# Kernel optimization log

Hardware: AMD Instinct MI355X
Metric: run time of the kernel (lower is better)

## Reference

```python
import jax, jax.numpy as jnp
import numpy as np

NEG = -1e30  # acts as -inf for logcumsumexp but keeps grads finite


def setup_inputs() -> dict:
    key = jax.random.key(0)
    k1, k2, k3 = jax.random.split(key, 3)
    B, N, L = 2048, 8192, 512
    y_pred_scores = jax.random.normal(k1, (B, N), dtype=jnp.float32)
    idx = jax.random.randint(k2, (B, L), 0, N)
    # ragged valid lengths in [L//2, L]; positions >= length are padded with -1
    lengths = jax.random.randint(k3, (B, 1), L // 2, L + 1)
    pos = jnp.arange(L)[None, :]
    y_true_seqs = jnp.where(pos < lengths, idx, -1).astype(jnp.int64)
    return {"y_pred_scores": y_pred_scores, "y_true_seqs": y_true_seqs}


def reference(y_pred_scores, y_true_seqs):
    # sanitize (torch_sanitize)
    s = jnp.nan_to_num(y_pred_scores, nan=0.0, posinf=1e6, neginf=-1e6)
    mask = y_true_seqs != -1                      # [B, L]
    idx = jnp.clip(y_true_seqs, 0, s.shape[1] - 1)
    g = jnp.take_along_axis(s, idx, axis=1)       # [B, L] gathered scores
    # Removing padded entries then flip+logcumsumexp+flip == suffix logsumexp
    # over the sequence with padded positions contributing exp(NEG)=0.
    gm = jnp.where(mask, g, NEG)
    log_den = jax.lax.cumlogsumexp(gm[:, ::-1], axis=1)[:, ::-1]  # [B, L]
    ll = jnp.where(mask, g - log_den, 0.0).sum(axis=1)            # [B]
    used = jnp.any(mask, axis=1)                                  # [B]
    total_ll = jnp.where(used, ll, 0.0).sum()
    n_used = used.sum().astype(s.dtype)
    return jnp.where(n_used > 0, -total_ll / n_used, jnp.zeros((), s.dtype))
```

## Files before the change

kernel.cpp:

```cpp
#include <hip/hip_runtime.h>

#define NEGV (-1e30f)

__global__ __launch_bounds__(256) void listnet_row_kernel(
    const float* __restrict__ scores,
    const int*   __restrict__ seqs,
    float2*      __restrict__ part,
    int N, int L)
{
    const int b = blockIdx.x;
    const float* srow = scores + (size_t)b * N;
    const int2*  irow = (const int2*)(seqs + (size_t)b * L);

    const int t    = threadIdx.x;
    const int lane = t & 63;
    const int wv   = t >> 6;

    int2 ii = irow[t];
    bool v0 = (ii.x != -1), v1 = (ii.y != -1);
    int  c0 = min(max(ii.x, 0), N - 1);
    int  c1 = min(max(ii.y, 0), N - 1);
    float g0 = srow[c0];
    float g1 = srow[c1];
    g0 = isnan(g0) ? 0.f : fminf(fmaxf(g0, -1e6f), 1e6f);
    g1 = isnan(g1) ? 0.f : fminf(fmaxf(g1, -1e6f), 1e6f);
    float x0 = v0 ? g0 : NEGV;
    float x1 = v1 ? g1 : NEGV;

    float mx = fmaxf(x0, x1);
    #pragma unroll
    for (int off = 32; off; off >>= 1)
        mx = fmaxf(mx, __shfl_xor(mx, off, 64));
    __shared__ float wmax[4];
    if (lane == 0) wmax[wv] = mx;
    __syncthreads();
    const float M = fmaxf(fmaxf(wmax[0], wmax[1]), fmaxf(wmax[2], wmax[3]));

    float e0 = __expf(x0 - M);
    float e1 = __expf(x1 - M);
    float S  = e0 + e1;
    #pragma unroll
    for (int off = 1; off < 64; off <<= 1) {
        float o = __shfl_down(S, off, 64);
        S += (lane + off < 64) ? o : 0.f;
    }
    __shared__ float wtot[4];
    if (lane == 0) wtot[wv] = S;
    float Safter = __shfl_down(S, 1, 64);
    if (lane == 63) Safter = 0.f;
    __syncthreads();
    float above = 0.f;
    if (wv < 3) above += wtot[wv + 1];
    if (wv < 2) above += wtot[wv + 2];
    if (wv < 1) above += wtot[wv + 3];
    const float A = Safter + above;

    float s1 = e1 + A;
    float s0 = e0 + s1;
    float ll = 0.f;
    if (v1) ll += x1 - (M + __logf(s1));
    if (v0) ll += x0 - (M + __logf(s0));

    #pragma unroll
    for (int off = 32; off; off >>= 1)
        ll += __shfl_down(ll, off, 64);
    __shared__ float lsum[4];
    if (lane == 0) lsum[wv] = ll;
    __syncthreads();
    if (t == 0) {
        bool used = (M > -1e29f);
        float2 r;
        r.x = used ? (lsum[0] + lsum[1] + lsum[2] + lsum[3]) : 0.f;
        r.y = used ? 1.f : 0.f;
        part[b] = r;
    }
}

__global__ __launch_bounds__(64) void listnet_finalize_kernel(
    const float2* __restrict__ part, float* __restrict__ out, int B)
{
    const int t = threadIdx.x;
    float tot = 0.f, cnt = 0.f;
    for (int i = t; i < B; i += 64) {
        float2 p = part[i];
        tot += p.x;
        cnt += p.y;
    }
    #pragma unroll
    for (int off = 32; off; off >>= 1) {
        tot += __shfl_down(tot, off, 64);
        cnt += __shfl_down(cnt, off, 64);
    }
    if (t == 0)
        out[0] = (cnt > 0.f) ? (-tot / cnt) : 0.f;
}

extern "C" void kernel_launch(void* const* d_in, const int* in_sizes, int n_in,
                              void* d_out, int out_size, void* d_ws, size_t ws_size,
                              hipStream_t stream) {
    const float* scores = (const float*)d_in[0];
    const int*   seqs   = (const int*)d_in[1];
    float*       out    = (float*)d_out;
    float2*      part   = (float2*)d_ws;

    const int L = 512;
    const int B = in_sizes[1] / L;
    const int N = in_sizes[0] / B;

    listnet_row_kernel<<<B, 256, 0, stream>>>(scores, seqs, part, N, L);
    listnet_finalize_kernel<<<1, 64, 0, stream>>>(part, out, B);
}
```

Baseline: 100.4 us.

## Process one row per wavefront and fuse finalize via last-block atomic counter

Each wavefront now handles a whole row with 8 elements per lane, so the block-level shared-memory reductions and __syncthreads barriers go away and only wave shuffles remain. The separate finalize kernel is replaced by an atomic counter: the last wave to finish reduces the partial results and writes the output. This removes one kernel launch but adds a hipMemsetAsync to reset the counter and puts the serial tail reduction inside the main kernel. The workload is gather-latency bound, so any gain depends on whether fewer barriers and more independent loads per thread improve latency hiding.

```diff
diff --git a/kernel.cpp b/kernel.cpp
--- a/kernel.cpp
+++ b/kernel.cpp
@@ -2,97 +2,99 @@
 
 #define NEGV (-1e30f)
 
-__global__ __launch_bounds__(256) void listnet_row_kernel(
+__global__ __launch_bounds__(256) void listnet_fused_kernel(
     const float* __restrict__ scores,
     const int*   __restrict__ seqs,
     float2*      __restrict__ part,
-    int N, int L)
+    int*         __restrict__ counter,
+    float*       __restrict__ out,
+    int N, int L, int B)
 {
-    const int b = blockIdx.x;
-    const float* srow = scores + (size_t)b * N;
-    const int2*  irow = (const int2*)(seqs + (size_t)b * L);
+    const int lane = threadIdx.x & 63;
+    const int wv   = threadIdx.x >> 6;
+    const int row  = blockIdx.x * 4 + wv;
+    if (row >= B) return;
 
-    const int t    = threadIdx.x;
-    const int lane = t & 63;
-    const int wv   = t >> 6;
+    const float* srow  = scores + (size_t)row * N;
+    const int4*  irow4 = (const int4*)(seqs + (size_t)row * L);
 
-    int2 ii = irow[t];
-    bool v0 = (ii.x != -1), v1 = (ii.y != -1);
-    int  c0 = min(max(ii.x, 0), N - 1);
-    int  c1 = min(max(ii.y, 0), N - 1);
-    float g0 = srow[c0];
-    float g1 = srow[c1];
-    g0 = isnan(g0) ? 0.f : fminf(fmaxf(g0, -1e6f), 1e6f);
-    g1 = isnan(g1) ? 0.f : fminf(fmaxf(g1, -1e6f), 1e6f);
-    float x0 = v0 ? g0 : NEGV;
-    float x1 = v1 ? g1 : NEGV;
+    int4 ia = irow4[lane * 2];
+    int4 ib = irow4[lane * 2 + 1];
+    int idx[8] = {ia.x, ia.y, ia.z, ia.w, ib.x, ib.y, ib.z, ib.w};
 
-    float mx = fmaxf(x0, x1);
+    float x[8];
+    float mloc = NEGV;
+    #pragma unroll
+    for (int j = 0; j < 8; ++j) {
+        bool v = (idx[j] != -1);
+        int  c = min(max(idx[j], 0), N - 1);
+        float g = srow[c];
+        g = isnan(g) ? 0.f : fminf(fmaxf(g, -1e6f), 1e6f);
+        x[j] = v ? g : NEGV;
+        mloc = fmaxf(mloc, x[j]);
+    }
+
+    float M = mloc;
     #pragma unroll
     for (int off = 32; off; off >>= 1)
-        mx = fmaxf(mx, __shfl_xor(mx, off, 64));
-    __shared__ float wmax[4];
-    if (lane == 0) wmax[wv] = mx;
-    __syncthreads();
-    const float M = fmaxf(fmaxf(wmax[0], wmax[1]), fmaxf(wmax[2], wmax[3]));
+        M = fmaxf(M, __shfl_xor(M, off, 64));
 
-    float e0 = __expf(x0 - M);
-    float e1 = __expf(x1 - M);
-    float S  = e0 + e1;
+    float suf[8];
+    float run = 0.f;
+    #pragma unroll
+    for (int j = 7; j >= 0; --j) {
+        run += __expf(x[j] - M);
+        suf[j] = run;
+    }
+
+    float S = run;
     #pragma unroll
     for (int off = 1; off < 64; off <<= 1) {
         float o = __shfl_down(S, off, 64);
         S += (lane + off < 64) ? o : 0.f;
     }
-    __shared__ float wtot[4];
-    if (lane == 0) wtot[wv] = S;
-    float Safter = __shfl_down(S, 1, 64);
-    if (lane == 63) Safter = 0.f;
-    __syncthreads();
-    float above = 0.f;
-    if (wv < 3) above += wtot[wv + 1];
-    if (wv < 2) above += wtot[wv + 2];
-    if (wv < 1) above += wtot[wv + 3];
-    const float A = Safter + above;
+    float A = __shfl_down(S, 1, 64);
+    if (lane == 63) A = 0.f;
 
-    float s1 = e1 + A;
-    float s0 = e0 + s1;
     float ll = 0.f;
-    if (v1) ll += x1 - (M + __logf(s1));
-    if (v0) ll += x0 - (M + __logf(s0));
-
+    #pragma unroll
+    for (int j = 0; j < 8; ++j) {
+        if (idx[j] != -1)
+            ll += x[j] - (M + __logf(suf[j] + A));
+    }
     #pragma unroll
     for (int off = 32; off; off >>= 1)
         ll += __shfl_down(ll, off, 64);
-    __shared__ float lsum[4];
-    if (lane == 0) lsum[wv] = ll;
-    __syncthreads();
-    if (t == 0) {
+
+    int old = 0;
+    if (lane == 0) {
         bool used = (M > -1e29f);
         float2 r;
-        r.x = used ? (lsum[0] + lsum[1] + lsum[2] + lsum[3]) : 0.f;
+        r.x = used ? ll : 0.f;
         r.y = used ? 1.f : 0.f;
-        part[b] = r;
+        part[row] = r;
+        __threadfence();
+        old = atomicAdd(counter, 1);
     }
-}
+    old = __shfl(old, 0, 64);
 
-__global__ __launch_bounds__(64) void listnet_finalize_kernel(
-    const float2* __restrict__ part, float* __restrict__ out, int B)
-{
-    const int t = threadIdx.x;
-    float tot = 0.f, cnt = 0.f;
-    for (int i = t; i < B; i += 64) {
-        float2 p = part[i];
-        tot += p.x;
-        cnt += p.y;
+    if (old == B - 1) {
+        __threadfence();
+        const volatile float2* vp = (const volatile float2*)part;
+        float tot = 0.f, cnt = 0.f;
+        for (int i = lane; i < B; i += 64) {
+            float2 p; p.x = vp[i].x; p.y = vp[i].y;
+            tot += p.x;
+            cnt += p.y;
+        }
+        #pragma unroll
+        for (int off = 32; off; off >>= 1) {
+            tot += __shfl_down(tot, off, 64);
+            cnt += __shfl_down(cnt, off, 64);
+        }
+        if (lane == 0)
+            out[0] = (cnt > 0.f) ? (-tot / cnt) : 0.f;
     }
-    #pragma unroll
-    for (int off = 32; off; off >>= 1) {
-        tot += __shfl_down(tot, off, 64);
-        cnt += __shfl_down(cnt, off, 64);
-    }
-    if (t == 0)
-        out[0] = (cnt > 0.f) ? (-tot / cnt) : 0.f;
 }
 
 extern "C" void kernel_launch(void* const* d_in, const int* in_sizes, int n_in,
@@ -101,12 +103,15 @@
     const float* scores = (const float*)d_in[0];
     const int*   seqs   = (const int*)d_in[1];
     float*       out    = (float*)d_out;
-    float2*      part   = (float2*)d_ws;
 
     const int L = 512;
     const int B = in_sizes[1] / L;
     const int N = in_sizes[0] / B;
 
-    listnet_row_kernel<<<B, 256, 0, stream>>>(scores, seqs, part, N, L);
-    listnet_finalize_kernel<<<1, 64, 0, stream>>>(part, out, B);
+    float2* part    = (float2*)d_ws;
+    int*    counter = (int*)((char*)d_ws + (size_t)B * sizeof(float2));
+
+    hipMemsetAsync(counter, 0, sizeof(int), stream);
+    listnet_fused_kernel<<<(B + 3) / 4, 256, 0, stream>>>(
+        scores, seqs, part, counter, out, N, L, B);
 }
```

Measured after the change: 159.3 us. +58.6%, slower.
